# Performance work log

Measured on AMD Instinct MI355X. Metric: run time of the kernel, lower is better.

The kernel has to match this reference:

```python
import jax, jax.numpy as jnp
import numpy as np

N = 10000        # num_nodes
F_IN = 256       # dataset_num_features
H = 128          # hidden_channels
C_OUT = 40       # dataset_num_classes
L = 3            # num_layers
HEADS = 8
DH = H // HEADS  # per-head dim
E = 160000       # num edges (before self loops)
SCALE = 1.0 / float(np.sqrt(DH))


def setup_inputs() -> dict:
    key = jax.random.key(0)
    ks = jax.random.split(key, 8)
    s = lambda k, *sh: (jax.random.normal(k, sh, dtype=jnp.float32) * 0.05)
    return dict(
        edge_index=jax.random.randint(ks[0], (2, E), 0, N, dtype=jnp.int32),
        x_param=s(ks[1], N, F_IN),
        lin1_w=s(ks[2], F_IN, H),
        lin1_b=jnp.zeros((H,), jnp.float32),
        wq=s(ks[3], L, H, H),
        wk=s(ks[4], L, H, H),
        wv=s(ks[5], L, H, H),
        bq=jnp.zeros((L, H), jnp.float32),
        bk=jnp.zeros((L, H), jnp.float32),
        bv=jnp.zeros((L, H), jnp.float32),
        lin2_w=s(ks[6], H, C_OUT),
        lin2_b=jnp.zeros((C_OUT,), jnp.float32),
    )


def _gcn_norm(edge_index):
    # PyG gcn_norm: add self loops (weight 1), symmetric D^-1/2 A D^-1/2
    loops = jnp.arange(N, dtype=edge_index.dtype)
    row = jnp.concatenate([edge_index[0], loops])  # source j
    col = jnp.concatenate([edge_index[1], loops])  # target i
    deg = jax.ops.segment_sum(jnp.ones(row.shape, jnp.float32), col, num_segments=N)
    dis = jnp.where(deg > 0, jax.lax.rsqrt(jnp.maximum(deg, 1e-12)), 0.0)
    return row, col, dis[row] * dis[col]


def _restricted_softmax(score):
    # softmax with an implicit extra logit at `margin=0`
    m = jnp.maximum(jnp.max(score, axis=-1, keepdims=True), 0.0)
    e = jnp.exp(score - m)
    return e / (jnp.sum(e, axis=-1, keepdims=True) + jnp.exp(-m))


def _forward(edge_index, x_param, lin1_w, lin1_b, wq, wk, wv, bq, bk, bv, lin2_w, lin2_b):
    row, col, norm = _gcn_norm(edge_index)
    # dropouts are eval-mode no-ops
    x = jax.nn.relu(x_param @ lin1_w + lin1_b)  # [N, H]
    x_all = x[:, None, :]                       # [N, 1, H]
    for l in range(L):
        t = x_all.shape[1]
        # project per-node first (linear commutes with per-edge gather)
        q = (x_all[:, -1] @ wq[l] + bq[l]).reshape(N, HEADS, DH)      # query from latest state
        k = (x_all @ wk[l] + bk[l]).reshape(N, t, HEADS, DH)          # keys over full history
        v = (x_all @ wv[l] + bv[l]).reshape(N, t, HEADS, DH)
        qe = q[col]   # [Etot, heads, dh]   (x_i)
        ke = k[row]   # [Etot, t, heads, dh] (x_j)
        ve = v[row]
        score = jnp.einsum('ehd,ethd->eht', qe, ke) * SCALE
        attn = _restricted_softmax(score)        # attention-dropout is a no-op in eval
        msg = jnp.einsum('eht,ethd->ehd', attn, ve).reshape(-1, H) * norm[:, None]
        out = jax.ops.segment_sum(msg, col, num_segments=N)  # aggr='add'
        x = jax.nn.relu(out)
        x_all = jnp.concatenate([x_all, x[:, None, :]], axis=1)
    logits = x_all[:, -1] @ lin2_w + lin2_b
    return jax.nn.log_softmax(logits, axis=1)


def reference(edge_index, x_param, lin1_w, lin1_b, wq, wk, wv, bq, bk, bv, lin2_w, lin2_b):
    return _forward(edge_index, x_param, lin1_w, lin1_b, wq, wk, wv, bq, bk, bv, lin2_w, lin2_b)
```

## Files before the change

kernel.cpp:

```cpp
#include <hip/hip_runtime.h>
#include <math.h>

#define N_NODES 10000
#define F_IN_D  256
#define H_DIM   128
#define C_OUTD  40
#define NHEADS  8
#define NEDGES  160000
#define SCALE_F 0.25f
#define TILES_N 157
#define KVSZ    ((size_t)N_NODES * 3 * 256)

typedef __attribute__((ext_vector_type(8))) short bf16x8;
typedef __attribute__((ext_vector_type(4))) float f32x4;
typedef __attribute__((ext_vector_type(2))) float f32x2;

__device__ __forceinline__ unsigned short f2bf(float f) {
    unsigned int u = __float_as_uint(f);
    unsigned int r = (u + 0x7FFFu + ((u >> 16) & 1u)) >> 16;
    return (unsigned short)r;
}
__device__ __forceinline__ float bf2f(unsigned short h) {
    return __uint_as_float(((unsigned int)h) << 16);
}
__device__ __forceinline__ unsigned char f2fp8(float v) {
    int pk = __builtin_amdgcn_cvt_pk_fp8_f32(v, v, 0, false);
    return (unsigned char)(pk & 0xff);
}


__global__ __launch_bounds__(256) void k_prep1(const float* __restrict__ w1,
                                               unsigned short* __restrict__ W1T,
                                               int* __restrict__ degi) {
    int t = blockIdx.x * 256 + threadIdx.x;
    if (t < 8192) {
        float4 v = *(const float4*)(w1 + 4 * t);
        int e = 4 * t;
        #pragma unroll
        for (int i = 0; i < 4; ++i) {
            int k = (e + i) >> 7, n = (e + i) & 127;
            W1T[n * 256 + k] = f2bf(((const float*)&v)[i]);
        }
    } else if (t < 10692) {
        int idx = (t - 8192) * 4;
        *(int4*)&degi[idx] = make_int4(0, 0, 0, 0);
    }
}


__device__ __forceinline__ void lin1_block(int bid, int ct0, const float* __restrict__ X,
                                           const unsigned short* __restrict__ W1T,
                                           const float* __restrict__ b1,
                                           unsigned short* __restrict__ X0, int nct) {
    int tid = threadIdx.x;
    int wid = tid >> 6, lane = tid & 63;
    int m = lane & 15, quad = lane >> 4;
    int rowA = bid * 64 + wid * 16 + m;
    int rowc = rowA < N_NODES ? rowA : N_NODES - 1;
    bf16x8 af[8];
    const float* ap = X + (size_t)rowc * F_IN_D + quad * 8;
    #pragma unroll
    for (int s = 0; s < 8; ++s) {
        float4 lo = *(const float4*)(ap + s * 32);
        float4 hi = *(const float4*)(ap + s * 32 + 4);
        union { unsigned short u[8]; bf16x8 v; } pk;
        pk.u[0] = f2bf(lo.x); pk.u[1] = f2bf(lo.y);
        pk.u[2] = f2bf(lo.z); pk.u[3] = f2bf(lo.w);
        pk.u[4] = f2bf(hi.x); pk.u[5] = f2bf(hi.y);
        pk.u[6] = f2bf(hi.z); pk.u[7] = f2bf(hi.w);
        af[s] = pk.v;
    }
    int row0 = bid * 64 + wid * 16 + quad * 4;
    for (int ct = ct0; ct < ct0 + nct; ++ct) {
        int col = ct * 16 + m;
        const unsigned short* bp = W1T + (size_t)col * F_IN_D + quad * 8;
        f32x4 acc = {0.f, 0.f, 0.f, 0.f};
        #pragma unroll
        for (int s = 0; s < 8; ++s) {
            bf16x8 bfr = __builtin_bit_cast(bf16x8, *(const uint4*)(bp + s * 32));
            acc = __builtin_amdgcn_mfma_f32_16x16x32_bf16(af[s], bfr, acc, 0, 0, 0);
        }
        float bb = b1[col];
        #pragma unroll
        for (int rg = 0; rg < 4; ++rg) {
            int r = row0 + rg;
            if (r < N_NODES)
                X0[(size_t)r * H_DIM + col] = f2bf(fmaxf(acc[rg] + bb, 0.f));
        }
    }
}

__device__ __forceinline__ void qkv_block(int mi, int rt,
                                          const unsigned short* __restrict__ XHb,
                                          const unsigned short* __restrict__ WTq_l,
                                          const unsigned short* __restrict__ WTk_l,
                                          const unsigned short* __restrict__ WTv_l,
                                          const float* __restrict__ bq_l,
                                          const float* __restrict__ bk_l,
                                          const float* __restrict__ bv_l,
                                          unsigned short* __restrict__ Qb,
                                          unsigned char* __restrict__ KVb,
                                          int hasQ, int qslice, int nK, int sbase,
                                          int cp0, int nct) {
    int tid = threadIdx.x;
    int wid = tid >> 6, lane = tid & 63;
    int m = lane & 15, quad = lane >> 4;
    const unsigned short* WT; const float* bias; int slice, mode;
    if (hasQ && mi == 0) { WT = WTq_l; bias = bq_l; slice = qslice; mode = 0; }
    else {
        int j = mi - hasQ;
        if (j < nK) { WT = WTk_l; bias = bk_l; slice = sbase + j;      mode = 1; }
        else        { WT = WTv_l; bias = bv_l; slice = sbase + j - nK; mode = 2; }
    }
    const unsigned short* A = XHb + (size_t)slice * N_NODES * H_DIM;
    int rowA = rt * 64 + wid * 16 + m;
    bf16x8 af[4];
    const unsigned short* ap = A + (size_t)rowA * H_DIM + quad * 8;
    #pragma unroll
    for (int s = 0; s < 4; ++s)
        af[s] = __builtin_bit_cast(bf16x8, *(const uint4*)(ap + s * 32));
    int row0 = rt * 64 + wid * 16 + quad * 4;
    int vofs = (mode == 2) ? 8 : 0;
    for (int cp = cp0; cp < cp0 + nct; ++cp) {
        int colA = cp * 32 + m;
        int colB = colA + 16;
        const unsigned short* bpA = WT + (size_t)colA * H_DIM + quad * 8;
        const unsigned short* bpB = WT + (size_t)colB * H_DIM + quad * 8;
        bf16x8 bA[4], bB[4];
        #pragma unroll
        for (int s = 0; s < 4; ++s) {
            bA[s] = __builtin_bit_cast(bf16x8, *(const uint4*)(bpA + s * 32));
            bB[s] = __builtin_bit_cast(bf16x8, *(const uint4*)(bpB + s * 32));
        }
        f32x4 accA = {0.f, 0.f, 0.f, 0.f};
        f32x4 accB = {0.f, 0.f, 0.f, 0.f};
        #pragma unroll
        for (int s = 0; s < 4; ++s) {
            accA = __builtin_amdgcn_mfma_f32_16x16x32_bf16(af[s], bA[s], accA, 0, 0, 0);
            accB = __builtin_amdgcn_mfma_f32_16x16x32_bf16(af[s], bB[s], accB, 0, 0, 0);
        }
        float bbA = bias[colA], bbB = bias[colB];
        #pragma unroll
        for (int rg = 0; rg < 4; ++rg) {
            int r = row0 + rg;
            if (r < N_NODES) {
                float vA = accA[rg] + bbA;
                float vB = accB[rg] + bbB;
                if (mode == 0) {
                    Qb[(size_t)r * H_DIM + colA] = f2bf(vA * SCALE_F);
                    Qb[(size_t)r * H_DIM + colB] = f2bf(vB * SCALE_F);
                } else {
                    size_t nb = ((size_t)r * 3 + slice) * 256;
                    KVb[nb + (colA >> 3) * 16 + (colA & 7) + vofs] = f2fp8(vA);
                    KVb[nb + (colB >> 3) * 16 + (colB & 7) + vofs] = f2fp8(vB);
                }
            }
        }
    }
}


template <int T>
__device__ __forceinline__ void kv_load(const uint4* __restrict__ KV, int r, int ci,
                                        uint4 (&kv)[T]) {
    const uint4* p = KV + (size_t)r * 48 + ci;
    #pragma unroll
    for (int s = 0; s < T; ++s) kv[s] = p[s * 16];
}

template <int T>
__device__ __forceinline__ void edge_accum(const uint4 (&kv)[T], const float (&q)[8],
                                           float nrm, float (&a)[8]) {
    float den = 1.f;
    float mv[8];
    #pragma unroll
    for (int i = 0; i < 8; ++i) mv[i] = 0.f;
    #pragma unroll
    for (int s = 0; s < T; ++s) {
        f32x2 k0 = __builtin_amdgcn_cvt_pk_f32_fp8(kv[s].x, false);
        f32x2 k1 = __builtin_amdgcn_cvt_pk_f32_fp8(kv[s].x, true);
        f32x2 k2 = __builtin_amdgcn_cvt_pk_f32_fp8(kv[s].y, false);
        f32x2 k3 = __builtin_amdgcn_cvt_pk_f32_fp8(kv[s].y, true);
        float p = q[0] * k0[0] + q[1] * k0[1] + q[2] * k1[0] + q[3] * k1[1]
                + q[4] * k2[0] + q[5] * k2[1] + q[6] * k3[0] + q[7] * k3[1];
        p += __shfl_xor(p, 1, 2);
        float w = __expf(p);
        den += w;
        f32x2 v0 = __builtin_amdgcn_cvt_pk_f32_fp8(kv[s].z, false);
        f32x2 v1 = __builtin_amdgcn_cvt_pk_f32_fp8(kv[s].z, true);
        f32x2 v2 = __builtin_amdgcn_cvt_pk_f32_fp8(kv[s].w, false);
        f32x2 v3 = __builtin_amdgcn_cvt_pk_f32_fp8(kv[s].w, true);
        mv[0] += w * v0[0]; mv[1] += w * v0[1];
        mv[2] += w * v1[0]; mv[3] += w * v1[1];
        mv[4] += w * v2[0]; mv[5] += w * v2[1];
        mv[6] += w * v3[0]; mv[7] += w * v3[1];
    }
    float ws = __fdividef(nrm, den);
    #pragma unroll
    for (int i = 0; i < 8; ++i) a[i] += ws * mv[i];
}

template <int T, bool LOGITS>
__device__ __forceinline__ void attn_block(int bid, const unsigned short* __restrict__ Q,
                                           const uint4* __restrict__ KV,
                                           const int* __restrict__ csr,
                                           const int* __restrict__ degi,
                                           unsigned int* __restrict__ Xout,
                                           const unsigned short* __restrict__ W2T,
                                           const float* __restrict__ b2,
                                           float* __restrict__ out) {
    int tid = threadIdx.x;
    int wid = tid >> 6, lane = tid & 63;
    int quarter = lane >> 4, ci = lane & 15;
    int n = bid * 4 + wid;

    int dn = degi[n];
    int cnt = dn + 1;
    if (cnt > 64) cnt = 64;
    float rn = rsqrtf((float)(dn + 1));
    int csrv = csr[(n << 6) + lane];
    int r = (lane < cnt - 1) ? csrv : n;
    int dr = degi[r];
    int   rAll = r;
    float nAll = (lane < cnt) ? rsqrtf((float)(dr + 1)) * rn : 0.f;

    float q[8];
    {
        uint4 qp = *(const uint4*)&Q[(size_t)n * H_DIM + ci * 8];
        q[0] = __uint_as_float(qp.x << 16);
        q[1] = __uint_as_float(qp.x & 0xffff0000u);
        q[2] = __uint_as_float(qp.y << 16);
        q[3] = __uint_as_float(qp.y & 0xffff0000u);
        q[4] = __uint_as_float(qp.z << 16);
        q[5] = __uint_as_float(qp.z & 0xffff0000u);
        q[6] = __uint_as_float(qp.w << 16);
        q[7] = __uint_as_float(qp.w & 0xffff0000u);
    }
    int nq = (cnt + 3) >> 2;
    float a[8];
    #pragma unroll
    for (int i = 0; i < 8; ++i) a[i] = 0.f;

    auto rowN = [&](int j4) { return __shfl(rAll, j4 < 63 ? j4 : 63, 64); };
    auto nrmN = [&](int j4) { return __shfl(nAll, j4 < 63 ? j4 : 63, 64); };

    uint4 kv0[T], kv1[T], kv2[T], kv3[T];
    kv_load<T>(KV, rowN(quarter), ci, kv0);
    kv_load<T>(KV, rowN(4 + quarter), ci, kv1);
    kv_load<T>(KV, rowN(8 + quarter), ci, kv2);
    kv_load<T>(KV, rowN(12 + quarter), ci, kv3);

    int j = 0;
    for (;;) {
        edge_accum<T>(kv0, q, nrmN(j * 4 + quarter), a);
        if (++j >= nq) break;
        kv_load<T>(KV, rowN((j + 3) * 4 + quarter), ci, kv0);
        edge_accum<T>(kv1, q, nrmN(j * 4 + quarter), a);
        if (++j >= nq) break;
        kv_load<T>(KV, rowN((j + 3) * 4 + quarter), ci, kv1);
        edge_accum<T>(kv2, q, nrmN(j * 4 + quarter), a);
        if (++j >= nq) break;
        kv_load<T>(KV, rowN((j + 3) * 4 + quarter), ci, kv2);
        edge_accum<T>(kv3, q, nrmN(j * 4 + quarter), a);
        if (++j >= nq) break;
        kv_load<T>(KV, rowN((j + 3) * 4 + quarter), ci, kv3);
    }

    #pragma unroll
    for (int i = 0; i < 8; ++i) {
        a[i] += __shfl_xor(a[i], 16, 64);
        a[i] += __shfl_xor(a[i], 32, 64);
    }

    if (!LOGITS) {
        if (quarter == 0) {
            uint4 o;
            o.x = ((unsigned int)f2bf(fmaxf(a[1], 0.f)) << 16) | (unsigned int)f2bf(fmaxf(a[0], 0.f));
            o.y = ((unsigned int)f2bf(fmaxf(a[3], 0.f)) << 16) | (unsigned int)f2bf(fmaxf(a[2], 0.f));
            o.z = ((unsigned int)f2bf(fmaxf(a[5], 0.f)) << 16) | (unsigned int)f2bf(fmaxf(a[4], 0.f));
            o.w = ((unsigned int)f2bf(fmaxf(a[7], 0.f)) << 16) | (unsigned int)f2bf(fmaxf(a[6], 0.f));
            *(uint4*)&Xout[(size_t)n * 64 + ci * 4] = o;
        }
        return;
    }

    float x[8];
    #pragma unroll
    for (int i = 0; i < 8; ++i) x[i] = fmaxf(a[i], 0.f);
    float lg[10];
    #pragma unroll
    for (int jj = 0; jj < 10; ++jj) {
        int c = quarter * 10 + jj;
        uint4 w = *(const uint4*)&W2T[c * H_DIM + ci * 8];
        float p = x[0] * bf2f((unsigned short)(w.x & 0xffff))
                + x[1] * bf2f((unsigned short)(w.x >> 16))
                + x[2] * bf2f((unsigned short)(w.y & 0xffff))
                + x[3] * bf2f((unsigned short)(w.y >> 16))
                + x[4] * bf2f((unsigned short)(w.z & 0xffff))
                + x[5] * bf2f((unsigned short)(w.z >> 16))
                + x[6] * bf2f((unsigned short)(w.w & 0xffff))
                + x[7] * bf2f((unsigned short)(w.w >> 16));
        #pragma unroll
        for (int o = 1; o < 16; o <<= 1) p += __shfl_xor(p, o, 16);
        lg[jj] = p + b2[c];
    }
    float mx = lg[0];
    #pragma unroll
    for (int jj = 1; jj < 10; ++jj) mx = fmaxf(mx, lg[jj]);
    mx = fmaxf(mx, __shfl_xor(mx, 16, 64));
    mx = fmaxf(mx, __shfl_xor(mx, 32, 64));
    float sm = 0.f;
    #pragma unroll
    for (int jj = 0; jj < 10; ++jj) sm += __expf(lg[jj] - mx);
    sm += __shfl_xor(sm, 16, 64);
    sm += __shfl_xor(sm, 32, 64);
    float lse = mx + __logf(sm);
    if (ci == 0) {
        float* op = out + (size_t)n * C_OUTD + quarter * 10;
        #pragma unroll
        for (int jj = 0; jj < 10; ++jj) op[jj] = lg[jj] - lse;
    }
}


__global__ __launch_bounds__(256) void k_degsc_lin1(const int* __restrict__ erow,
                                                    const int* __restrict__ ecol,
                                                    int* __restrict__ degi,
                                                    int* __restrict__ csr,
                                                    const float* __restrict__ X,
                                                    const unsigned short* __restrict__ W1T,
                                                    const float* __restrict__ b1,
                                                    unsigned short* __restrict__ X0,
                                                    const float* __restrict__ wq,
                                                    const float* __restrict__ wk,
                                                    const float* __restrict__ wv,
                                                    const float* __restrict__ w2,
                                                    unsigned short* __restrict__ WTq,
                                                    unsigned short* __restrict__ WTk,
                                                    unsigned short* __restrict__ WTv,
                                                    unsigned short* __restrict__ W2T,
                                                    int nct) {
    int b = blockIdx.x;
    if (b < 625) {
        int e = b * 256 + threadIdx.x;
        int c = ecol[e];
        int slot = atomicAdd(&degi[c], 1);
        if (slot < 64) csr[(c << 6) + slot] = erow[e];
        return;
    }
    if (b < 939) {
        int bid = b - 625;
        lin1_block(bid % TILES_N, (bid / TILES_N) * 4, X, W1T, b1, X0, nct);
        return;
    }
    int t = (b - 939) * 256 + threadIdx.x;
    if (t < 36864) {
        int mat = t >> 12;
        int l = mat / 3, ws = mat % 3;
        const float*    src = (ws == 0) ? wq  : (ws == 1) ? wk  : wv;
        unsigned short* dst = (ws == 0) ? WTq : (ws == 1) ? WTk : WTv;
        int e2 = (t & 4095) * 4;
        float4 v = *(const float4*)(src + l * 16384 + e2);
        #pragma unroll
        for (int i = 0; i < 4; ++i) {
            int k = (e2 + i) >> 7, n = (e2 + i) & 127;
            dst[l * 16384 + n * 128 + k] = f2bf(((const float*)&v)[i]);
        }
    } else if (t < 38144) {
        int e = (t - 36864) * 4;
        float4 v = *(const float4*)(w2 + e);
        #pragma unroll
        for (int i = 0; i < 4; ++i) {
            int ee = e + i;
            int k = ee / 40, c = ee - k * 40;
            W2T[c * H_DIM + k] = f2bf(((const float*)&v)[i]);
        }
    }
}

__global__ __launch_bounds__(256) void k_qkv(const unsigned short* __restrict__ XHb,
                                             const unsigned short* __restrict__ WTq_l,
                                             const unsigned short* __restrict__ WTk_l,
                                             const unsigned short* __restrict__ WTv_l,
                                             const float* __restrict__ bq_l,
                                             const float* __restrict__ bk_l,
                                             const float* __restrict__ bv_l,
                                             unsigned short* __restrict__ Qb,
                                             unsigned char* __restrict__ KVb,
                                             int qslice) {
    int half = blockIdx.x / (3 * TILES_N);
    int bb = blockIdx.x % (3 * TILES_N);
    qkv_block(bb / TILES_N, bb % TILES_N, XHb, WTq_l, WTk_l, WTv_l,
              bq_l, bk_l, bv_l, Qb, KVb, 1, qslice, 1, qslice, half * 2, 2);
}

template <int T>
__global__ __launch_bounds__(256) void k_attn_qkvold(const unsigned short* __restrict__ Q,
                                                     const uint4* __restrict__ KV,
                                                     const int* __restrict__ csr,
                                                     const int* __restrict__ degi,
                                                     unsigned int* __restrict__ Xout,
                                                     const unsigned short* __restrict__ XHb,
                                                     const unsigned short* __restrict__ WTk_l,
                                                     const unsigned short* __restrict__ WTv_l,
                                                     const float* __restrict__ bk_l,
                                                     const float* __restrict__ bv_l,
                                                     unsigned char* __restrict__ KVnext,
                                                     int nK) {
    if (blockIdx.x < 2500) {
        attn_block<T, false>(blockIdx.x, Q, KV, csr, degi, Xout,
                             nullptr, nullptr, nullptr);
        return;
    }
    int b = blockIdx.x - 2500;
    qkv_block(b / TILES_N, b % TILES_N, XHb, nullptr, WTk_l, WTv_l,
              nullptr, bk_l, bv_l, nullptr, KVnext, 0, 0, nK, 0, 0, 4);
}

__global__ __launch_bounds__(256) void k_attn_logits(const unsigned short* __restrict__ Q,
                                                     const uint4* __restrict__ KV,
                                                     const int* __restrict__ csr,
                                                     const int* __restrict__ degi,
                                                     const unsigned short* __restrict__ W2T,
                                                     const float* __restrict__ b2,
                                                     float* __restrict__ out) {
    attn_block<3, true>(blockIdx.x, Q, KV, csr, degi, nullptr, W2T, b2, out);
}


extern "C" void kernel_launch(void* const* d_in, const int* in_sizes, int n_in,
                              void* d_out, int out_size, void* d_ws, size_t ws_size,
                              hipStream_t stream) {
    const int*   ei      = (const int*)d_in[0];
    const int*   row     = ei;
    const int*   col     = ei + NEDGES;
    const float* x_param = (const float*)d_in[1];
    const float* lin1_w  = (const float*)d_in[2];
    const float* lin1_b  = (const float*)d_in[3];
    const float* wq      = (const float*)d_in[4];
    const float* wk      = (const float*)d_in[5];
    const float* wv      = (const float*)d_in[6];
    const float* bq      = (const float*)d_in[7];
    const float* bk      = (const float*)d_in[8];
    const float* bv      = (const float*)d_in[9];
    const float* lin2_w  = (const float*)d_in[10];
    const float* lin2_b  = (const float*)d_in[11];
    float*       out     = (float*)d_out;

    char* wbase = (char*)d_ws;
    size_t off = 0;
    auto alloc = [&](size_t bytes) -> void* {
        off = (off + 255) & ~(size_t)255;
        void* p = wbase + off;
        off += bytes;
        return p;
    };
    int*            degi     = (int*)           alloc((size_t)N_NODES * 4);
    int*            csr      = (int*)           alloc((size_t)N_NODES * 64 * 4);
    unsigned short* W1T      = (unsigned short*)alloc((size_t)H_DIM * F_IN_D * 2);
    unsigned short* WTq      = (unsigned short*)alloc((size_t)3 * H_DIM * H_DIM * 2);
    unsigned short* WTk      = (unsigned short*)alloc((size_t)3 * H_DIM * H_DIM * 2);
    unsigned short* WTv      = (unsigned short*)alloc((size_t)3 * H_DIM * H_DIM * 2);
    unsigned short* W2T      = (unsigned short*)alloc((size_t)C_OUTD * H_DIM * 2);
    unsigned short* XHb      = (unsigned short*)alloc((size_t)3 * N_NODES * H_DIM * 2);
    unsigned short* Qb       = (unsigned short*)alloc((size_t)N_NODES * H_DIM * 2);
    unsigned char*  KVb      = (unsigned char*) alloc(2 * KVSZ);

    k_prep1<<<42, 256, 0, stream>>>(lin1_w, W1T, degi);

    k_degsc_lin1<<<1089, 256, 0, stream>>>(row, col, degi, csr,
                                           x_param, W1T, lin1_b, XHb,
                                           wq, wk, wv, lin2_w,
                                           WTq, WTk, WTv, W2T, 4);

    k_qkv<<<6 * TILES_N, 256, 0, stream>>>(
        XHb, WTq, WTk, WTv, bq, bk, bv, Qb, KVb, 0);

    unsigned int* X1 = (unsigned int*)(XHb + (size_t)1 * N_NODES * H_DIM);
    unsigned int* X2 = (unsigned int*)(XHb + (size_t)2 * N_NODES * H_DIM);

    k_attn_qkvold<1><<<2500 + 2 * TILES_N, 256, 0, stream>>>(
        Qb, (const uint4*)KVb, csr, degi, X1,
        XHb, WTk + 16384, WTv + 16384, bk + H_DIM, bv + H_DIM,
        KVb + KVSZ, 1);

    k_qkv<<<6 * TILES_N, 256, 0, stream>>>(
        XHb, WTq + 16384, WTk + 16384, WTv + 16384,
        bq + H_DIM, bk + H_DIM, bv + H_DIM, Qb, KVb + KVSZ, 1);

    k_attn_qkvold<2><<<2500 + 4 * TILES_N, 256, 0, stream>>>(
        Qb, (const uint4*)(KVb + KVSZ), csr, degi, X2,
        XHb, WTk + 2 * 16384, WTv + 2 * 16384, bk + 2 * H_DIM, bv + 2 * H_DIM,
        KVb, 2);

    k_qkv<<<6 * TILES_N, 256, 0, stream>>>(
        XHb, WTq + 2 * 16384, WTk + 2 * 16384, WTv + 2 * 16384,
        bq + 2 * H_DIM, bk + 2 * H_DIM, bv + 2 * H_DIM, Qb, KVb, 2);

    k_attn_logits<<<2500, 256, 0, stream>>>(Qb, (const uint4*)KVb, csr, degi,
                                            W2T, lin2_b, out);
}
```

Before: 214.6 us.

## Move old-history K/V projections into QKV kernels and shrink attention blocks

The K/V projections of older history states for later layers are no longer fused into the attention kernels. They now run inside the QKV projection launches, and a third KV buffer is added so each layer has its own. Attention kernels become pure 64-thread, one-node-per-block launches with no GEMM tail. The aim is to even out load balance and block shape in the gather-heavy attention kernels, at the cost of more KV workspace and heavier QKV launches.

```diff
diff --git a/kernel.cpp b/kernel.cpp
--- a/kernel.cpp
+++ b/kernel.cpp
@@ -201,18 +201,16 @@
 }
 
 template <int T, bool LOGITS>
-__device__ __forceinline__ void attn_block(int bid, const unsigned short* __restrict__ Q,
-                                           const uint4* __restrict__ KV,
-                                           const int* __restrict__ csr,
-                                           const int* __restrict__ degi,
-                                           unsigned int* __restrict__ Xout,
-                                           const unsigned short* __restrict__ W2T,
-                                           const float* __restrict__ b2,
-                                           float* __restrict__ out) {
-    int tid = threadIdx.x;
-    int wid = tid >> 6, lane = tid & 63;
+__device__ __forceinline__ void attn_node(int n, const unsigned short* __restrict__ Q,
+                                          const uint4* __restrict__ KV,
+                                          const int* __restrict__ csr,
+                                          const int* __restrict__ degi,
+                                          unsigned int* __restrict__ Xout,
+                                          const unsigned short* __restrict__ W2T,
+                                          const float* __restrict__ b2,
+                                          float* __restrict__ out) {
+    int lane = threadIdx.x & 63;
     int quarter = lane >> 4, ci = lane & 15;
-    int n = bid * 4 + wid;
 
     int dn = degi[n];
     int cnt = dn + 1;
@@ -378,53 +376,99 @@
     }
 }
 
-__global__ __launch_bounds__(256) void k_qkv(const unsigned short* __restrict__ XHb,
-                                             const unsigned short* __restrict__ WTq_l,
-                                             const unsigned short* __restrict__ WTk_l,
-                                             const unsigned short* __restrict__ WTv_l,
-                                             const float* __restrict__ bq_l,
-                                             const float* __restrict__ bk_l,
-                                             const float* __restrict__ bv_l,
-                                             unsigned short* __restrict__ Qb,
-                                             unsigned char* __restrict__ KVb,
-                                             int qslice) {
+__global__ __launch_bounds__(256) void k_qkv0_old(const unsigned short* __restrict__ XHb,
+                                                  const unsigned short* __restrict__ WTq,
+                                                  const unsigned short* __restrict__ WTk,
+                                                  const unsigned short* __restrict__ WTv,
+                                                  const float* __restrict__ bq,
+                                                  const float* __restrict__ bk,
+                                                  const float* __restrict__ bv,
+                                                  unsigned short* __restrict__ Qb,
+                                                  unsigned char* __restrict__ B0,
+                                                  unsigned char* __restrict__ B1,
+                                                  unsigned char* __restrict__ B2) {
+    int b = blockIdx.x;
+    if (b < 6 * TILES_N) {
+        int half = b / (3 * TILES_N);
+        int bb = b % (3 * TILES_N);
+        qkv_block(bb / TILES_N, bb % TILES_N, XHb, WTq, WTk, WTv, bq, bk, bv,
+                  Qb, B0, 1, 0, 1, 0, half * 2, 2);
+        return;
+    }
+    int idx = b - 6 * TILES_N;
+    int layer = idx / (2 * TILES_N);
+    int rr = idx % (2 * TILES_N);
+    int mi = rr / TILES_N;
+    int rt = rr % TILES_N;
+    int woff = (layer + 1) * 16384;
+    unsigned char* dst = layer ? B2 : B1;
+    qkv_block(mi, rt, XHb, nullptr, WTk + woff, WTv + woff, nullptr,
+              bk + (layer + 1) * H_DIM, bv + (layer + 1) * H_DIM, nullptr,
+              dst, 0, 0, 1, 0, 0, 4);
+}
+
+__global__ __launch_bounds__(256) void k_qkvnew1_old2b(const unsigned short* __restrict__ XHb,
+                                                       const unsigned short* __restrict__ WTq,
+                                                       const unsigned short* __restrict__ WTk,
+                                                       const unsigned short* __restrict__ WTv,
+                                                       const float* __restrict__ bq,
+                                                       const float* __restrict__ bk,
+                                                       const float* __restrict__ bv,
+                                                       unsigned short* __restrict__ Qb,
+                                                       unsigned char* __restrict__ B1,
+                                                       unsigned char* __restrict__ B2) {
+    int b = blockIdx.x;
+    if (b < 6 * TILES_N) {
+        int half = b / (3 * TILES_N);
+        int bb = b % (3 * TILES_N);
+        qkv_block(bb / TILES_N, bb % TILES_N, XHb,
+                  WTq + 16384, WTk + 16384, WTv + 16384,
+                  bq + H_DIM, bk + H_DIM, bv + H_DIM,
+                  Qb, B1, 1, 1, 1, 1, half * 2, 2);
+        return;
+    }
+    int rr = b - 6 * TILES_N;
+    int mi = rr / TILES_N;
+    qkv_block(mi, rr % TILES_N, XHb, nullptr, WTk + 32768, WTv + 32768, nullptr,
+              bk + 2 * H_DIM, bv + 2 * H_DIM, nullptr,
+              B2, 0, 0, 1, 1, 0, 4);
+}
+
+__global__ __launch_bounds__(256) void k_qkv2(const unsigned short* __restrict__ XHb,
+                                              const unsigned short* __restrict__ WTq,
+                                              const unsigned short* __restrict__ WTk,
+                                              const unsigned short* __restrict__ WTv,
+                                              const float* __restrict__ bq,
+                                              const float* __restrict__ bk,
+                                              const float* __restrict__ bv,
+                                              unsigned short* __restrict__ Qb,
+                                              unsigned char* __restrict__ B2) {
     int half = blockIdx.x / (3 * TILES_N);
     int bb = blockIdx.x % (3 * TILES_N);
-    qkv_block(bb / TILES_N, bb % TILES_N, XHb, WTq_l, WTk_l, WTv_l,
-              bq_l, bk_l, bv_l, Qb, KVb, 1, qslice, 1, qslice, half * 2, 2);
+    qkv_block(bb / TILES_N, bb % TILES_N, XHb,
+              WTq + 32768, WTk + 32768, WTv + 32768,
+              bq + 2 * H_DIM, bk + 2 * H_DIM, bv + 2 * H_DIM,
+              Qb, B2, 1, 2, 1, 2, half * 2, 2);
 }
 
 template <int T>
-__global__ __launch_bounds__(256) void k_attn_qkvold(const unsigned short* __restrict__ Q,
-                                                     const uint4* __restrict__ KV,
-                                                     const int* __restrict__ csr,
-                                                     const int* __restrict__ degi,
-                                                     unsigned int* __restrict__ Xout,
-                                                     const unsigned short* __restrict__ XHb,
-                                                     const unsigned short* __restrict__ WTk_l,
-                                                     const unsigned short* __restrict__ WTv_l,
-                                                     const float* __restrict__ bk_l,
-                                                     const float* __restrict__ bv_l,
-                                                     unsigned char* __restrict__ KVnext,
-                                                     int nK) {
-    if (blockIdx.x < 2500) {
-        attn_block<T, false>(blockIdx.x, Q, KV, csr, degi, Xout,
-                             nullptr, nullptr, nullptr);
-        return;
-    }
-    int b = blockIdx.x - 2500;
-    qkv_block(b / TILES_N, b % TILES_N, XHb, nullptr, WTk_l, WTv_l,
-              nullptr, bk_l, bv_l, nullptr, KVnext, 0, 0, nK, 0, 0, 4);
-}
-
-__global__ __launch_bounds__(256) void k_attn_logits(const unsigned short* __restrict__ Q,
-                                                     const uint4* __restrict__ KV,
-                                                     const int* __restrict__ csr,
-                                                     const int* __restrict__ degi,
-                                                     const unsigned short* __restrict__ W2T,
-                                                     const float* __restrict__ b2,
-                                                     float* __restrict__ out) {
-    attn_block<3, true>(blockIdx.x, Q, KV, csr, degi, nullptr, W2T, b2, out);
+__global__ __launch_bounds__(64) void k_attn_pure(const unsigned short* __restrict__ Q,
+                                                  const uint4* __restrict__ KV,
+                                                  const int* __restrict__ csr,
+                                                  const int* __restrict__ degi,
+                                                  unsigned int* __restrict__ Xout) {
+    attn_node<T, false>(blockIdx.x, Q, KV, csr, degi, Xout,
+                        nullptr, nullptr, nullptr);
+}
+
+__global__ __launch_bounds__(64) void k_attn_logits(const unsigned short* __restrict__ Q,
+                                                    const uint4* __restrict__ KV,
+                                                    const int* __restrict__ csr,
+                                                    const int* __restrict__ degi,
+                                                    const unsigned short* __restrict__ W2T,
+                                                    const float* __restrict__ b2,
+                                                    float* __restrict__ out) {
+    attn_node<3, true>(blockIdx.x, Q, KV, csr, degi, nullptr, W2T, b2, out);
 }
 
 
@@ -464,7 +508,10 @@
     unsigned short* W2T      = (unsigned short*)alloc((size_t)C_OUTD * H_DIM * 2);
     unsigned short* XHb      = (unsigned short*)alloc((size_t)3 * N_NODES * H_DIM * 2);
     unsigned short* Qb       = (unsigned short*)alloc((size_t)N_NODES * H_DIM * 2);
-    unsigned char*  KVb      = (unsigned char*) alloc(2 * KVSZ);
+    unsigned char*  KVb      = (unsigned char*) alloc(3 * KVSZ);
+    unsigned char*  B0 = KVb;
+    unsigned char*  B1 = KVb + KVSZ;
+    unsigned char*  B2 = KVb + 2 * KVSZ;
 
     k_prep1<<<42, 256, 0, stream>>>(lin1_w, W1T, degi);
 
@@ -473,30 +520,22 @@
                                            wq, wk, wv, lin2_w,
                                            WTq, WTk, WTv, W2T, 4);
 
-    k_qkv<<<6 * TILES_N, 256, 0, stream>>>(
-        XHb, WTq, WTk, WTv, bq, bk, bv, Qb, KVb, 0);
+    k_qkv0_old<<<6 * TILES_N + 4 * TILES_N, 256, 0, stream>>>(
+        XHb, WTq, WTk, WTv, bq, bk, bv, Qb, B0, B1, B2);
 
     unsigned int* X1 = (unsigned int*)(XHb + (size_t)1 * N_NODES * H_DIM);
     unsigned int* X2 = (unsigned int*)(XHb + (size_t)2 * N_NODES * H_DIM);
 
-    k_attn_qkvold<1><<<2500 + 2 * TILES_N, 256, 0, stream>>>(
-        Qb, (const uint4*)KVb, csr, degi, X1,
-        XHb, WTk + 16384, WTv + 16384, bk + H_DIM, bv + H_DIM,
-        KVb + KVSZ, 1);
-
-    k_qkv<<<6 * TILES_N, 256, 0, stream>>>(
-        XHb, WTq + 16384, WTk + 16384, WTv + 16384,
-        bq + H_DIM, bk + H_DIM, bv + H_DIM, Qb, KVb + KVSZ, 1);
-
-    k_attn_qkvold<2><<<2500 + 4 * TILES_N, 256, 0, stream>>>(
-        Qb, (const uint4*)(KVb + KVSZ), csr, degi, X2,
-        XHb, WTk + 2 * 16384, WTv + 2 * 16384, bk + 2 * H_DIM, bv + 2 * H_DIM,
-        KVb, 2);
-
-    k_qkv<<<6 * TILES_N, 256, 0, stream>>>(
-        XHb, WTq + 2 * 16384, WTk + 2 * 16384, WTv + 2 * 16384,
-        bq + 2 * H_DIM, bk + 2 * H_DIM, bv + 2 * H_DIM, Qb, KVb, 2);
-
-    k_attn_logits<<<2500, 256, 0, stream>>>(Qb, (const uint4*)KVb, csr, degi,
-                                            W2T, lin2_b, out);
-}
+    k_attn_pure<1><<<N_NODES, 64, 0, stream>>>(Qb, (const uint4*)B0, csr, degi, X1);
+
+    k_qkvnew1_old2b<<<6 * TILES_N + 2 * TILES_N, 256, 0, stream>>>(
+        XHb, WTq, WTk, WTv, bq, bk, bv, Qb, B1, B2);
+
+    k_attn_pure<2><<<N_NODES, 64, 0, stream>>>(Qb, (const uint4*)B1, csr, degi, X2);
+
+    k_qkv2<<<6 * TILES_N, 256, 0, stream>>>(XHb, WTq, WTk, WTv, bq, bk, bv,
+                                            Qb, B2);
+
+    k_attn_logits<<<N_NODES, 64, 0, stream>>>(Qb, (const uint4*)B2, csr, degi,
+                                              W2T, lin2_b, out);
+}
```

After: 211.9 us, median of 2. No clear change (-1.3%).
